# Optimization experiments

Hardware: AMD Instinct MI355X
Metric: run time of the kernel (lower is better)

The kernel has to match this reference:

```python
import jax, jax.numpy as jnp
import numpy as np

N_NODES = 50000
NEG_SLOPE = 0.2  # PyG GATConv default


def gat_layer(x, src, dst, W, a_src, a_dst, b, concat):
    """PyG-style GATConv (eval mode, self-loops already in src/dst).
    x: [N, Fin], W: [Fin, H*C], a_src/a_dst: [H, C], b: [H*C] or [C]."""
    N = x.shape[0]
    H, C = a_src.shape
    h = (x @ W).reshape(N, H, C)                      # [N,H,C]
    alpha_s = jnp.einsum('nhc,hc->nh', h, a_src)      # [N,H]
    alpha_d = jnp.einsum('nhc,hc->nh', h, a_dst)
    e = jax.nn.leaky_relu(alpha_s[src] + alpha_d[dst], NEG_SLOPE)  # [E,H]
    # segment softmax over incoming edges of each dst node
    m = jax.ops.segment_max(e, dst, num_segments=N)   # [N,H]
    e = jnp.exp(e - m[dst])
    denom = jax.ops.segment_sum(e, dst, num_segments=N)  # [N,H]
    msg = e[:, :, None] * h[src]                      # [E,H,C] (largest intermediate)
    out = jax.ops.segment_sum(msg, dst, num_segments=N)
    out = out / jnp.maximum(denom[:, :, None], 1e-16) # [N,H,C]
    out = out.reshape(N, H * C) if concat else out.mean(axis=1)
    return out + b


def setup_inputs() -> dict:
    key = jax.random.key(0)
    ks = jax.random.split(key, 10)
    N, E = N_NODES, 1600000
    Fin, Chid, Cout, H = 3, 32, 16, 4
    s = lambda *sh: 1.0 / np.sqrt(sh[-1])
    return {
        'x': jax.random.normal(ks[0], (N, Fin), dtype=jnp.float32),
        'edge_index': jax.random.randint(ks[1], (2, E), 0, N, dtype=jnp.int64),
        'W1': jax.random.normal(ks[2], (Fin, H * Chid), dtype=jnp.float32) * s(Fin),
        'att_src1': jax.random.normal(ks[3], (H, Chid), dtype=jnp.float32) * s(Chid),
        'att_dst1': jax.random.normal(ks[4], (H, Chid), dtype=jnp.float32) * s(Chid),
        'b1': jnp.zeros((H * Chid,), dtype=jnp.float32),
        'W2': jax.random.normal(ks[5], (H * Chid, Cout), dtype=jnp.float32) * s(H * Chid),
        'att_src2': jax.random.normal(ks[6], (1, Cout), dtype=jnp.float32) * s(Cout),
        'att_dst2': jax.random.normal(ks[7], (1, Cout), dtype=jnp.float32) * s(Cout),
        'b2': jnp.zeros((Cout,), dtype=jnp.float32),
    }


def reference(x, edge_index, W1, att_src1, att_dst1, b1, W2, att_src2, att_dst2, b2):
    N = x.shape[0]
    loops = jnp.arange(N, dtype=edge_index.dtype)
    src = jnp.concatenate([edge_index[0], loops])
    dst = jnp.concatenate([edge_index[1], loops])
    h = gat_layer(x, src, dst, W1, att_src1, att_dst1, b1, concat=True)  # [N,128]
    h = jax.nn.elu(h)  # dropout is identity in eval mode
    out = gat_layer(h, src, dst, W2, att_src2, att_dst2, b2, concat=False)  # [N,16]
    return out
```

## Files before the change

### kernel.cpp

```cpp
#include <hip/hip_runtime.h>

#define LRELU(v) ((v) > 0.f ? (v) : 0.2f * (v))
#define MAXNB 512
#define BCAP 8192
#define WCAP (BCAP + 128)
#define MS_CHUNK 8192

__global__ void __launch_bounds__(256) k_h1(const float* __restrict__ x,
                                            const float* __restrict__ W1,
                                            const float* __restrict__ aws,
                                            const float* __restrict__ awd,
                                            const int* __restrict__ ei,
                                            float* __restrict__ rec,
                                            float* __restrict__ ad1,
                                            int* __restrict__ gcur,
                                            int* __restrict__ flag, int nb, int N) {
    int t = threadIdx.x;
    if (blockIdx.x == 0) {
        for (int i = t; i < nb; i += 256) gcur[i] = i * BCAP;
        if (t < 64) {
            int a = ei[2 * t + 1];
            int b = ei[2 * (t + 64) + 1];
            unsigned long long any = __ballot((a | b) != 0);
            if (t == 0) *flag = (any == 0ull) ? 1 : 0;
        }
    }
    int n = blockIdx.x * 2 + (t >> 7);
    int f = t & 127;
    if (n >= N) return;
    float x0 = x[n * 3 + 0], x1 = x[n * 3 + 1], x2 = x[n * 3 + 2];
    float h = fmaf(x0, W1[f], fmaf(x1, W1[128 + f], x2 * W1[256 + f]));
    float ps = h * aws[f];
    float pd = h * awd[f];
#pragma unroll
    for (int m = 1; m < 32; m <<= 1) {
        ps += __shfl_xor(ps, m);
        pd += __shfl_xor(pd, m);
    }
    int head = f >> 5;
    if ((f & 31) == 0) {
        rec[n * 8 + head] = ps;
        ad1[n * 4 + head] = pd;
    }
    if (f < 3) rec[n * 8 + 4 + f] = x[n * 3 + f];
}

__global__ void __launch_bounds__(256) k_msplit(const int* __restrict__ ei, long long E,
                                                const int* __restrict__ flag,
                                                int* __restrict__ gcur,
                                                unsigned* __restrict__ bstage) {
    __shared__ unsigned stage[MS_CHUNK];
    __shared__ int h[MAXNB], lbase[MAXNB], lcur[MAXNB];
    int t = threadIdx.x;
    for (int i = t; i < MAXNB; i += 256) h[i] = 0;
    __syncthreads();
    long long beg = (long long)blockIdx.x * MS_CHUNK;
    int cnt = (int)min((long long)MS_CHUNK, E - beg);
    int is64 = *flag;
    for (int k = t; k < cnt; k += 256) {
        long long i = beg + k;
        int s, d;
        if (is64) {
            s = (int)((const long long*)ei)[i];
            d = (int)((const long long*)ei)[E + i];
        } else {
            s = ei[i];
            d = ei[E + i];
        }
        stage[k] = (unsigned)s | ((unsigned)d << 16);
        atomicAdd(&h[d >> 7], 1);
    }
    __syncthreads();
    for (int b = t; b < MAXNB; b += 256) {
        lcur[b] = 0;
        if (h[b]) lbase[b] = atomicAdd(&gcur[b], h[b]);
    }
    __syncthreads();
    for (int k = t; k < cnt; k += 256) {
        unsigned pk = stage[k];
        int b = (int)(pk >> 23);
        int idx = lbase[b] + atomicAdd(&lcur[b], 1);
        if (idx < (b + 1) * BCAP) bstage[idx] = pk;
    }
}

__global__ void __launch_bounds__(256) k_bucket(const unsigned* __restrict__ bstage,
                                                const int* __restrict__ gcur,
                                                int* __restrict__ beg,
                                                int* __restrict__ endo,
                                                int* __restrict__ ssrc, int N) {
    __shared__ int nc[128];
    __shared__ int sscan[128];
    __shared__ int lcur[128];
    int b = blockIdx.x, t = threadIdx.x;
    if (t < 128) nc[t] = 0;
    __syncthreads();
    int base = b * BCAP;
    int c = min(gcur[b], (b + 1) * BCAP) - base;
    for (int i = t; i < c; i += 256)
        atomicAdd(&nc[(bstage[base + i] >> 16) & 127], 1);
    __syncthreads();
    int node = b * 128 + (t & 127);
    int v = 0;
    if (t < 128) {
        v = (node < N) ? nc[t] + 1 : 0;
        sscan[t] = v;
    }
    __syncthreads();
#pragma unroll
    for (int off = 1; off < 128; off <<= 1) {
        int add = (t < 128 && t >= off) ? sscan[t - off] : 0;
        __syncthreads();
        if (t < 128) sscan[t] += add;
        __syncthreads();
    }
    int sbase = b * WCAP;
    if (t < 128 && node < N) {
        int o = sbase + sscan[t] - v;
        beg[node] = o;
        endo[node] = o + v;
        ssrc[o] = node;
        lcur[t] = o + 1;
    }
    __syncthreads();
    for (int i = t; i < c; i += 256) {
        unsigned pk = bstage[base + i];
        int p = atomicAdd(&lcur[(pk >> 16) & 127], 1);
        ssrc[p] = (int)(pk & 0xFFFFu);
    }
}

__global__ void __launch_bounds__(256) k_gat1w(const float* __restrict__ rec,
                                               const float* __restrict__ ad1,
                                               const int* __restrict__ beg,
                                               const int* __restrict__ endo,
                                               const int* __restrict__ ssrc,
                                               const float* __restrict__ W1,
                                               const float* __restrict__ b1,
                                               const float* __restrict__ W2,
                                               const float* __restrict__ aws2,
                                               const float* __restrict__ awd2,
                                               float* __restrict__ h2w,
                                               float* __restrict__ as2,
                                               float* __restrict__ ad2, int N) {
    __shared__ float sW1[384], sb1[128], sW2[128 * 16];
    __shared__ float shx[16][132];
    int t = threadIdx.x;
    for (int i = t; i < 384; i += 256) sW1[i] = W1[i];
    if (t < 128) sb1[t] = b1[t];
    for (int i = t; i < 2048; i += 256) sW2[i] = W2[i];

    int nl = t >> 4;
    int g = t & 15;
    int n = blockIdx.x * 16 + nl;

    float t0_0 = 0.f, t1_0 = 0.f, t2_0 = 0.f, ds_0 = 0.f;
    float t0_1 = 0.f, t1_1 = 0.f, t2_1 = 0.f, ds_1 = 0.f;
    float t0_2 = 0.f, t1_2 = 0.f, t2_2 = 0.f, ds_2 = 0.f;
    float t0_3 = 0.f, t1_3 = 0.f, t2_3 = 0.f, ds_3 = 0.f;
    if (n < N) {
        int e0 = beg[n], e1 = endo[n];
        const float4 adv = *(const float4*)(ad1 + (size_t)n * 4);
        for (int e = e0 + g; e < e1; e += 16) {
            int s = ssrc[e];
            const float4 a4 = *(const float4*)(rec + (size_t)s * 8);
            const float4 x4 = *(const float4*)(rec + (size_t)s * 8 + 4);
            float w;
            w = __expf(LRELU(a4.x + adv.x));
            ds_0 += w; t0_0 = fmaf(w, x4.x, t0_0); t1_0 = fmaf(w, x4.y, t1_0); t2_0 = fmaf(w, x4.z, t2_0);
            w = __expf(LRELU(a4.y + adv.y));
            ds_1 += w; t0_1 = fmaf(w, x4.x, t0_1); t1_1 = fmaf(w, x4.y, t1_1); t2_1 = fmaf(w, x4.z, t2_1);
            w = __expf(LRELU(a4.z + adv.z));
            ds_2 += w; t0_2 = fmaf(w, x4.x, t0_2); t1_2 = fmaf(w, x4.y, t1_2); t2_2 = fmaf(w, x4.z, t2_2);
            w = __expf(LRELU(a4.w + adv.w));
            ds_3 += w; t0_3 = fmaf(w, x4.x, t0_3); t1_3 = fmaf(w, x4.y, t1_3); t2_3 = fmaf(w, x4.z, t2_3);
        }
    }
#pragma unroll
    for (int msk = 1; msk < 16; msk <<= 1) {
        t0_0 += __shfl_xor(t0_0, msk); t1_0 += __shfl_xor(t1_0, msk);
        t2_0 += __shfl_xor(t2_0, msk); ds_0 += __shfl_xor(ds_0, msk);
        t0_1 += __shfl_xor(t0_1, msk); t1_1 += __shfl_xor(t1_1, msk);
        t2_1 += __shfl_xor(t2_1, msk); ds_1 += __shfl_xor(ds_1, msk);
        t0_2 += __shfl_xor(t0_2, msk); t1_2 += __shfl_xor(t1_2, msk);
        t2_2 += __shfl_xor(t2_2, msk); ds_2 += __shfl_xor(ds_2, msk);
        t0_3 += __shfl_xor(t0_3, msk); t1_3 += __shfl_xor(t1_3, msk);
        t2_3 += __shfl_xor(t2_3, msk); ds_3 += __shfl_xor(ds_3, msk);
    }
    int hs = g >> 2;
    float u0 = hs == 0 ? t0_0 : hs == 1 ? t0_1 : hs == 2 ? t0_2 : t0_3;
    float u1 = hs == 0 ? t1_0 : hs == 1 ? t1_1 : hs == 2 ? t1_2 : t1_3;
    float u2 = hs == 0 ? t2_0 : hs == 1 ? t2_1 : hs == 2 ? t2_2 : t2_3;
    float dsv = hs == 0 ? ds_0 : hs == 1 ? ds_1 : hs == 2 ? ds_2 : ds_3;
    float ui = 1.f / fmaxf(dsv, 1e-16f);

    __syncthreads();
    int f0 = g * 8;
#pragma unroll
    for (int j = 0; j < 8; ++j) {
        int f = f0 + j;
        float o = fmaf(fmaf(u0, sW1[f], fmaf(u1, sW1[128 + f], u2 * sW1[256 + f])), ui, sb1[f]);
        shx[nl][f] = (o > 0.f) ? o : __expf(o) - 1.f;
    }
    __syncthreads();

    int c = g;
    const float4* hr4 = (const float4*)shx[nl];
    float acc = 0.f;
#pragma unroll 8
    for (int k4 = 0; k4 < 32; ++k4) {
        float4 hv = hr4[k4];
        acc = fmaf(hv.x, sW2[(k4 * 4 + 0) * 16 + c], acc);
        acc = fmaf(hv.y, sW2[(k4 * 4 + 1) * 16 + c], acc);
        acc = fmaf(hv.z, sW2[(k4 * 4 + 2) * 16 + c], acc);
        acc = fmaf(hv.w, sW2[(k4 * 4 + 3) * 16 + c], acc);
    }
    if (n < N) {
        h2w[(size_t)n * 16 + c] = acc;
        float ps = acc * aws2[c];
        float pd = acc * awd2[c];
#pragma unroll
        for (int m = 1; m < 16; m <<= 1) {
            ps += __shfl_xor(ps, m);
            pd += __shfl_xor(pd, m);
        }
        if (c == 0) {
            as2[n] = ps;
            ad2[n] = pd;
        }
    }
}

__global__ void __launch_bounds__(256) k_gat2(const float* __restrict__ h2w,
                                              const float* __restrict__ as2,
                                              const float* __restrict__ ad2,
                                              const int* __restrict__ beg,
                                              const int* __restrict__ endo,
                                              const int* __restrict__ ssrc,
                                              const float* __restrict__ b2,
                                              float* __restrict__ out, int N) {
    int t = threadIdx.x;
    int nl = t >> 4, g = t & 15;
    int n = blockIdx.x * 16 + nl;
    if (n >= N) return;
    int slot = g >> 2, c4 = g & 3;
    int e0 = beg[n], e1 = endo[n];
    float ad = ad2[n];

    float4 acc = {0.f, 0.f, 0.f, 0.f};
    float ds = 0.f;
    for (int e = e0 + slot; e < e1; e += 4) {
        int s = ssrc[e];
        float w = __expf(LRELU(as2[s] + ad));
        ds += w;
        const float4 hv = *(const float4*)(h2w + (size_t)s * 16 + c4 * 4);
        acc.x = fmaf(w, hv.x, acc.x);
        acc.y = fmaf(w, hv.y, acc.y);
        acc.z = fmaf(w, hv.z, acc.z);
        acc.w = fmaf(w, hv.w, acc.w);
    }
#pragma unroll
    for (int msk = 4; msk < 16; msk <<= 1) {
        acc.x += __shfl_xor(acc.x, msk);
        acc.y += __shfl_xor(acc.y, msk);
        acc.z += __shfl_xor(acc.z, msk);
        acc.w += __shfl_xor(acc.w, msk);
        ds += __shfl_xor(ds, msk);
    }
    if (slot == 0) {
        float inv = 1.f / fmaxf(ds, 1e-16f);
        float4 bq = ((const float4*)b2)[c4];
        float4 o;
        o.x = fmaf(acc.x, inv, bq.x);
        o.y = fmaf(acc.y, inv, bq.y);
        o.z = fmaf(acc.z, inv, bq.z);
        o.w = fmaf(acc.w, inv, bq.w);
        *(float4*)(out + (size_t)n * 16 + c4 * 4) = o;
    }
}

extern "C" void kernel_launch(void* const* d_in, const int* in_sizes, int n_in,
                              void* d_out, int out_size, void* d_ws, size_t ws_size,
                              hipStream_t stream) {
    const float* x    = (const float*)d_in[0];
    const int*   ei   = (const int*)d_in[1];
    const float* W1   = (const float*)d_in[2];
    const float* aws1 = (const float*)d_in[3];
    const float* awd1 = (const float*)d_in[4];
    const float* b1   = (const float*)d_in[5];
    const float* W2   = (const float*)d_in[6];
    const float* aws2 = (const float*)d_in[7];
    const float* awd2 = (const float*)d_in[8];
    const float* b2   = (const float*)d_in[9];
    float* out = (float*)d_out;

    const int N = in_sizes[0] / 3;
    const long long E = in_sizes[1] / 2;
    const int NB = (N + 127) / 128;

    char* w = (char*)d_ws;
    auto alloc = [&](size_t bytes) {
        char* p = w;
        w += (bytes + 255) & ~(size_t)255;
        return p;
    };
    float*    rec    = (float*)alloc((size_t)N * 8 * 4);
    float*    ad1    = (float*)alloc((size_t)N * 4 * 4);
    float*    h2w    = (float*)alloc((size_t)N * 16 * 4);
    float*    as2    = (float*)alloc((size_t)N * 4);
    float*    ad2    = (float*)alloc((size_t)N * 4);
    int*      beg    = (int*)alloc((size_t)N * 4);
    int*      endo   = (int*)alloc((size_t)N * 4);
    int*      ssrc   = (int*)alloc((size_t)NB * WCAP * 4);
    unsigned* bstage = (unsigned*)alloc((size_t)NB * BCAP * 4);
    int*      gcur   = (int*)alloc((size_t)NB * 4);
    int*      flag   = (int*)alloc(4);

    k_h1<<<(N + 1) / 2, 256, 0, stream>>>(x, W1, aws1, awd1, ei, rec, ad1,
                                          gcur, flag, NB, N);
    k_msplit<<<(int)((E + MS_CHUNK - 1) / MS_CHUNK), 256, 0, stream>>>(ei, E, flag, gcur, bstage);
    k_bucket<<<NB, 256, 0, stream>>>(bstage, gcur, beg, endo, ssrc, N);
    k_gat1w<<<(N + 15) / 16, 256, 0, stream>>>(rec, ad1, beg, endo, ssrc, W1, b1,
                                               W2, aws2, awd2, h2w, as2, ad2, N);
    k_gat2<<<(N + 15) / 16, 256, 0, stream>>>(h2w, as2, ad2, beg, endo, ssrc, b2, out, N);
}
```

Baseline: 111.0 us.

## Fuse bucket CSR build with layer-1 GAT aggregation in one kernel

Merges the per-bucket CSR construction kernel and the layer-1 attention/aggregation plus W2 projection kernel into one 512-thread kernel per 128-node bucket. Each block builds its bucket's segment offsets in shared memory, then processes its 128 nodes in four tiles of 32. This removes a kernel launch and the global round trip for beg/endo. In exchange, parallelism drops to one block per bucket (about 391 blocks), and each block runs serially through more work with extra syncs.

```diff
diff --git a/kernel.cpp b/kernel.cpp
--- a/kernel.cpp
+++ b/kernel.cpp
@@ -84,23 +84,39 @@
     }
 }
 
-__global__ void __launch_bounds__(256) k_bucket(const unsigned* __restrict__ bstage,
-                                                const int* __restrict__ gcur,
-                                                int* __restrict__ beg,
-                                                int* __restrict__ endo,
-                                                int* __restrict__ ssrc, int N) {
-    __shared__ int nc[128];
-    __shared__ int sscan[128];
-    __shared__ int lcur[128];
+__global__ void __launch_bounds__(512) k_b1(const unsigned* __restrict__ bstage,
+                                            const int* __restrict__ gcur,
+                                            const float* __restrict__ rec,
+                                            const float* __restrict__ ad1,
+                                            const float* __restrict__ W1,
+                                            const float* __restrict__ b1,
+                                            const float* __restrict__ W2,
+                                            const float* __restrict__ aws2,
+                                            const float* __restrict__ awd2,
+                                            int* __restrict__ beg,
+                                            int* __restrict__ endo,
+                                            int* __restrict__ ssrc,
+                                            float* __restrict__ h2w,
+                                            float* __restrict__ as2,
+                                            float* __restrict__ ad2, int N) {
+    __shared__ int nc[128], sscan[128], lcur[128], begL[128], endL[128];
+    __shared__ float sW1[384], sb1[128], sW2[128 * 16];
+    __shared__ float shx[32][132];
+
     int b = blockIdx.x, t = threadIdx.x;
-    if (t < 128) nc[t] = 0;
-    __syncthreads();
+    int node0 = b * 128;
     int base = b * BCAP;
-    int c = min(gcur[b], (b + 1) * BCAP) - base;
-    for (int i = t; i < c; i += 256)
+    int cnt = min(gcur[b], base + BCAP) - base;
+
+    for (int i = t; i < 384; i += 512) sW1[i] = W1[i];
+    for (int i = t; i < 2048; i += 512) sW2[i] = W2[i];
+    if (t < 128) { sb1[t] = b1[t]; nc[t] = 0; }
+    __syncthreads();
+
+    for (int i = t; i < cnt; i += 512)
         atomicAdd(&nc[(bstage[base + i] >> 16) & 127], 1);
     __syncthreads();
-    int node = b * 128 + (t & 127);
+    int node = node0 + (t & 127);
     int v = 0;
     if (t < 128) {
         v = (node < N) ? nc[t] + 1 : 0;
@@ -119,115 +135,100 @@
         int o = sbase + sscan[t] - v;
         beg[node] = o;
         endo[node] = o + v;
+        begL[t] = o;
+        endL[t] = o + v;
         ssrc[o] = node;
         lcur[t] = o + 1;
     }
     __syncthreads();
-    for (int i = t; i < c; i += 256) {
+    for (int i = t; i < cnt; i += 512) {
         unsigned pk = bstage[base + i];
         int p = atomicAdd(&lcur[(pk >> 16) & 127], 1);
         ssrc[p] = (int)(pk & 0xFFFFu);
     }
-}
-
-__global__ void __launch_bounds__(256) k_gat1w(const float* __restrict__ rec,
-                                               const float* __restrict__ ad1,
-                                               const int* __restrict__ beg,
-                                               const int* __restrict__ endo,
-                                               const int* __restrict__ ssrc,
-                                               const float* __restrict__ W1,
-                                               const float* __restrict__ b1,
-                                               const float* __restrict__ W2,
-                                               const float* __restrict__ aws2,
-                                               const float* __restrict__ awd2,
-                                               float* __restrict__ h2w,
-                                               float* __restrict__ as2,
-                                               float* __restrict__ ad2, int N) {
-    __shared__ float sW1[384], sb1[128], sW2[128 * 16];
-    __shared__ float shx[16][132];
-    int t = threadIdx.x;
-    for (int i = t; i < 384; i += 256) sW1[i] = W1[i];
-    if (t < 128) sb1[t] = b1[t];
-    for (int i = t; i < 2048; i += 256) sW2[i] = W2[i];
+    __syncthreads();
 
     int nl = t >> 4;
     int g = t & 15;
-    int n = blockIdx.x * 16 + nl;
-
-    float t0_0 = 0.f, t1_0 = 0.f, t2_0 = 0.f, ds_0 = 0.f;
-    float t0_1 = 0.f, t1_1 = 0.f, t2_1 = 0.f, ds_1 = 0.f;
-    float t0_2 = 0.f, t1_2 = 0.f, t2_2 = 0.f, ds_2 = 0.f;
-    float t0_3 = 0.f, t1_3 = 0.f, t2_3 = 0.f, ds_3 = 0.f;
-    if (n < N) {
-        int e0 = beg[n], e1 = endo[n];
-        const float4 adv = *(const float4*)(ad1 + (size_t)n * 4);
-        for (int e = e0 + g; e < e1; e += 16) {
-            int s = ssrc[e];
-            const float4 a4 = *(const float4*)(rec + (size_t)s * 8);
-            const float4 x4 = *(const float4*)(rec + (size_t)s * 8 + 4);
-            float w;
-            w = __expf(LRELU(a4.x + adv.x));
-            ds_0 += w; t0_0 = fmaf(w, x4.x, t0_0); t1_0 = fmaf(w, x4.y, t1_0); t2_0 = fmaf(w, x4.z, t2_0);
-            w = __expf(LRELU(a4.y + adv.y));
-            ds_1 += w; t0_1 = fmaf(w, x4.x, t0_1); t1_1 = fmaf(w, x4.y, t1_1); t2_1 = fmaf(w, x4.z, t2_1);
-            w = __expf(LRELU(a4.z + adv.z));
-            ds_2 += w; t0_2 = fmaf(w, x4.x, t0_2); t1_2 = fmaf(w, x4.y, t1_2); t2_2 = fmaf(w, x4.z, t2_2);
-            w = __expf(LRELU(a4.w + adv.w));
-            ds_3 += w; t0_3 = fmaf(w, x4.x, t0_3); t1_3 = fmaf(w, x4.y, t1_3); t2_3 = fmaf(w, x4.z, t2_3);
-        }
-    }
-#pragma unroll
-    for (int msk = 1; msk < 16; msk <<= 1) {
-        t0_0 += __shfl_xor(t0_0, msk); t1_0 += __shfl_xor(t1_0, msk);
-        t2_0 += __shfl_xor(t2_0, msk); ds_0 += __shfl_xor(ds_0, msk);
-        t0_1 += __shfl_xor(t0_1, msk); t1_1 += __shfl_xor(t1_1, msk);
-        t2_1 += __shfl_xor(t2_1, msk); ds_1 += __shfl_xor(ds_1, msk);
-        t0_2 += __shfl_xor(t0_2, msk); t1_2 += __shfl_xor(t1_2, msk);
-        t2_2 += __shfl_xor(t2_2, msk); ds_2 += __shfl_xor(ds_2, msk);
-        t0_3 += __shfl_xor(t0_3, msk); t1_3 += __shfl_xor(t1_3, msk);
-        t2_3 += __shfl_xor(t2_3, msk); ds_3 += __shfl_xor(ds_3, msk);
-    }
-    int hs = g >> 2;
-    float u0 = hs == 0 ? t0_0 : hs == 1 ? t0_1 : hs == 2 ? t0_2 : t0_3;
-    float u1 = hs == 0 ? t1_0 : hs == 1 ? t1_1 : hs == 2 ? t1_2 : t1_3;
-    float u2 = hs == 0 ? t2_0 : hs == 1 ? t2_1 : hs == 2 ? t2_2 : t2_3;
-    float dsv = hs == 0 ? ds_0 : hs == 1 ? ds_1 : hs == 2 ? ds_2 : ds_3;
-    float ui = 1.f / fmaxf(dsv, 1e-16f);
-
-    __syncthreads();
-    int f0 = g * 8;
-#pragma unroll
-    for (int j = 0; j < 8; ++j) {
-        int f = f0 + j;
-        float o = fmaf(fmaf(u0, sW1[f], fmaf(u1, sW1[128 + f], u2 * sW1[256 + f])), ui, sb1[f]);
-        shx[nl][f] = (o > 0.f) ? o : __expf(o) - 1.f;
-    }
-    __syncthreads();
-
-    int c = g;
-    const float4* hr4 = (const float4*)shx[nl];
-    float acc = 0.f;
+#pragma unroll
+    for (int tile = 0; tile < 4; ++tile) {
+        int d = tile * 32 + nl;
+        int n = node0 + d;
+        float t0_0 = 0.f, t1_0 = 0.f, t2_0 = 0.f, ds_0 = 0.f;
+        float t0_1 = 0.f, t1_1 = 0.f, t2_1 = 0.f, ds_1 = 0.f;
+        float t0_2 = 0.f, t1_2 = 0.f, t2_2 = 0.f, ds_2 = 0.f;
+        float t0_3 = 0.f, t1_3 = 0.f, t2_3 = 0.f, ds_3 = 0.f;
+        if (n < N) {
+            int e0 = begL[d], e1 = endL[d];
+            const float4 adv = *(const float4*)(ad1 + (size_t)n * 4);
+            for (int e = e0 + g; e < e1; e += 16) {
+                int s = ssrc[e];
+                const float4 a4 = *(const float4*)(rec + (size_t)s * 8);
+                const float4 x4 = *(const float4*)(rec + (size_t)s * 8 + 4);
+                float w;
+                w = __expf(LRELU(a4.x + adv.x));
+                ds_0 += w; t0_0 = fmaf(w, x4.x, t0_0); t1_0 = fmaf(w, x4.y, t1_0); t2_0 = fmaf(w, x4.z, t2_0);
+                w = __expf(LRELU(a4.y + adv.y));
+                ds_1 += w; t0_1 = fmaf(w, x4.x, t0_1); t1_1 = fmaf(w, x4.y, t1_1); t2_1 = fmaf(w, x4.z, t2_1);
+                w = __expf(LRELU(a4.z + adv.z));
+                ds_2 += w; t0_2 = fmaf(w, x4.x, t0_2); t1_2 = fmaf(w, x4.y, t1_2); t2_2 = fmaf(w, x4.z, t2_2);
+                w = __expf(LRELU(a4.w + adv.w));
+                ds_3 += w; t0_3 = fmaf(w, x4.x, t0_3); t1_3 = fmaf(w, x4.y, t1_3); t2_3 = fmaf(w, x4.z, t2_3);
+            }
+        }
+#pragma unroll
+        for (int msk = 1; msk < 16; msk <<= 1) {
+            t0_0 += __shfl_xor(t0_0, msk); t1_0 += __shfl_xor(t1_0, msk);
+            t2_0 += __shfl_xor(t2_0, msk); ds_0 += __shfl_xor(ds_0, msk);
+            t0_1 += __shfl_xor(t0_1, msk); t1_1 += __shfl_xor(t1_1, msk);
+            t2_1 += __shfl_xor(t2_1, msk); ds_1 += __shfl_xor(ds_1, msk);
+            t0_2 += __shfl_xor(t0_2, msk); t1_2 += __shfl_xor(t1_2, msk);
+            t2_2 += __shfl_xor(t2_2, msk); ds_2 += __shfl_xor(ds_2, msk);
+            t0_3 += __shfl_xor(t0_3, msk); t1_3 += __shfl_xor(t1_3, msk);
+            t2_3 += __shfl_xor(t2_3, msk); ds_3 += __shfl_xor(ds_3, msk);
+        }
+        int hs = g >> 2;
+        float u0 = hs == 0 ? t0_0 : hs == 1 ? t0_1 : hs == 2 ? t0_2 : t0_3;
+        float u1 = hs == 0 ? t1_0 : hs == 1 ? t1_1 : hs == 2 ? t1_2 : t1_3;
+        float u2 = hs == 0 ? t2_0 : hs == 1 ? t2_1 : hs == 2 ? t2_2 : t2_3;
+        float dsv = hs == 0 ? ds_0 : hs == 1 ? ds_1 : hs == 2 ? ds_2 : ds_3;
+        float ui = 1.f / fmaxf(dsv, 1e-16f);
+
+        int f0 = g * 8;
+#pragma unroll
+        for (int j = 0; j < 8; ++j) {
+            int f = f0 + j;
+            float o = fmaf(fmaf(u0, sW1[f], fmaf(u1, sW1[128 + f], u2 * sW1[256 + f])), ui, sb1[f]);
+            shx[nl][f] = (o > 0.f) ? o : __expf(o) - 1.f;
+        }
+        __syncthreads();
+
+        int c = g;
+        const float4* hr4 = (const float4*)shx[nl];
+        float acc = 0.f;
 #pragma unroll 8
-    for (int k4 = 0; k4 < 32; ++k4) {
-        float4 hv = hr4[k4];
-        acc = fmaf(hv.x, sW2[(k4 * 4 + 0) * 16 + c], acc);
-        acc = fmaf(hv.y, sW2[(k4 * 4 + 1) * 16 + c], acc);
-        acc = fmaf(hv.z, sW2[(k4 * 4 + 2) * 16 + c], acc);
-        acc = fmaf(hv.w, sW2[(k4 * 4 + 3) * 16 + c], acc);
-    }
-    if (n < N) {
-        h2w[(size_t)n * 16 + c] = acc;
-        float ps = acc * aws2[c];
-        float pd = acc * awd2[c];
-#pragma unroll
-        for (int m = 1; m < 16; m <<= 1) {
-            ps += __shfl_xor(ps, m);
-            pd += __shfl_xor(pd, m);
-        }
-        if (c == 0) {
-            as2[n] = ps;
-            ad2[n] = pd;
-        }
+        for (int k4 = 0; k4 < 32; ++k4) {
+            float4 hv = hr4[k4];
+            acc = fmaf(hv.x, sW2[(k4 * 4 + 0) * 16 + c], acc);
+            acc = fmaf(hv.y, sW2[(k4 * 4 + 1) * 16 + c], acc);
+            acc = fmaf(hv.z, sW2[(k4 * 4 + 2) * 16 + c], acc);
+            acc = fmaf(hv.w, sW2[(k4 * 4 + 3) * 16 + c], acc);
+        }
+        if (n < N) {
+            h2w[(size_t)n * 16 + c] = acc;
+            float ps = acc * aws2[c];
+            float pd = acc * awd2[c];
+#pragma unroll
+            for (int m = 1; m < 16; m <<= 1) {
+                ps += __shfl_xor(ps, m);
+                pd += __shfl_xor(pd, m);
+            }
+            if (c == 0) {
+                as2[n] = ps;
+                ad2[n] = pd;
+            }
+        }
+        __syncthreads();
     }
 }
 
@@ -319,8 +320,7 @@
     k_h1<<<(N + 1) / 2, 256, 0, stream>>>(x, W1, aws1, awd1, ei, rec, ad1,
                                           gcur, flag, NB, N);
     k_msplit<<<(int)((E + MS_CHUNK - 1) / MS_CHUNK), 256, 0, stream>>>(ei, E, flag, gcur, bstage);
-    k_bucket<<<NB, 256, 0, stream>>>(bstage, gcur, beg, endo, ssrc, N);
-    k_gat1w<<<(N + 15) / 16, 256, 0, stream>>>(rec, ad1, beg, endo, ssrc, W1, b1,
-                                               W2, aws2, awd2, h2w, as2, ad2, N);
+    k_b1<<<NB, 512, 0, stream>>>(bstage, gcur, rec, ad1, W1, b1, W2,
+                                 aws2, awd2, beg, endo, ssrc, h2w, as2, ad2, N);
     k_gat2<<<(N + 15) / 16, 256, 0, stream>>>(h2w, as2, ad2, beg, endo, ssrc, b2, out, N);
 }
```

Result: slower. 116.0 us (+4.4%).
